# Kernel tuning notes

Measured on AMD Instinct MI355X. Metric: run time of the kernel, lower is better.

## Reference

```python
import jax, jax.numpy as jnp
import numpy as np

B, C, H, W = 8, 256, 64, 64
GROUPS = 32
EPS = 1e-6


def setup_inputs() -> dict:
    key = jax.random.key(0)
    ks = jax.random.split(key, 8)
    s = 0.02
    return {
        "x": jax.random.normal(ks[0], (B, C, H, W), dtype=jnp.float32),
        "gn_scale": jnp.ones((C,), jnp.float32),
        "gn_bias": jnp.zeros((C,), jnp.float32),
        "wq": jax.random.normal(ks[1], (C, C), jnp.float32) * s,
        "bq": jnp.zeros((C,), jnp.float32),
        "wk": jax.random.normal(ks[2], (C, C), jnp.float32) * s,
        "bk": jnp.zeros((C,), jnp.float32),
        "wv": jax.random.normal(ks[3], (C, C), jnp.float32) * s,
        "bv": jnp.zeros((C,), jnp.float32),
        "wproj": jax.random.normal(ks[4], (C, C), jnp.float32) * s,
        "bproj": jnp.zeros((C,), jnp.float32),
    }


def _group_norm(x, scale, bias):
    b, c, h, w = x.shape
    xg = x.reshape(b, GROUPS, c // GROUPS, h, w)
    mean = xg.mean(axis=(2, 3, 4), keepdims=True)
    var = xg.var(axis=(2, 3, 4), keepdims=True)
    xn = ((xg - mean) * jax.lax.rsqrt(var + EPS)).reshape(b, c, h, w)
    return xn * scale[None, :, None, None] + bias[None, :, None, None]


def _conv1x1(x, w, b):
    # 1x1 conv == channel-mixing matmul: w is [out_ch, in_ch]
    return jnp.einsum("oc,bchw->bohw", w, x) + b[None, :, None, None]


def reference(x, gn_scale, gn_bias, wq, bq, wk, bk, wv, bv, wproj, bproj):
    b, c, h, w = x.shape
    hn = _group_norm(x, gn_scale, gn_bias)
    q = _conv1x1(hn, wq, bq).reshape(b, c, h * w)  # [b,c,n]
    k = _conv1x1(hn, wk, bk).reshape(b, c, h * w)
    v = _conv1x1(hn, wv, bv).reshape(b, c, h * w)
    # scores[b,n,m] = <q[:, :, n], k[:, :, m]> * c^-0.5  (softmax over keys m)
    scale = jnp.asarray(c, x.dtype) ** -0.5
    attn = jax.nn.softmax(jnp.einsum("bcn,bcm->bnm", q, k) * scale, axis=2)
    # h_[b,c,n] = sum_m v[b,c,m] * attn[b,n,m]
    h_ = jnp.einsum("bcm,bnm->bcn", v, attn).reshape(b, c, h, w)
    h_ = _conv1x1(h_, wproj, bproj)
    return x + h_
```

## Files before the change

### kernel.cpp

```cpp
#include <hip/hip_runtime.h>

#define B_ 8
#define C_ 256
#define N_ 4096
#define G_ 32

typedef __bf16 bf16;
typedef __bf16 bf16x8 __attribute__((ext_vector_type(8)));
typedef float f32x4 __attribute__((ext_vector_type(4)));
typedef float f32x16 __attribute__((ext_vector_type(16)));
typedef long i64;
typedef long i64x2 __attribute__((ext_vector_type(2)));
typedef long i64x2a __attribute__((ext_vector_type(2), may_alias));
typedef int i32x8 __attribute__((ext_vector_type(8)));
typedef int i32x8a __attribute__((ext_vector_type(8), may_alias));
typedef unsigned int u32;
typedef unsigned char u8;
typedef unsigned short u16;
typedef unsigned long long u64;

__device__ __forceinline__ f32x4 mfma16(bf16x8 a, bf16x8 b, f32x4 c) {
    return __builtin_amdgcn_mfma_f32_16x16x32_bf16(a, b, c, 0, 0, 0);
}
__device__ __forceinline__ f32x16 mfma_mx(i32x8 a, i32x8 b, f32x16 c) {
    return __builtin_amdgcn_mfma_scale_f32_32x32x64_f8f6f4(
        a, b, c, 0 , 0 , 0, 0x7F7F7F7F, 0, 0x7F7F7F7F);
}

typedef __attribute__((address_space(1))) const void* gas_t;
typedef __attribute__((address_space(3))) void* las_t;
__device__ __forceinline__ void gl2lds16(const void* g, void* l) {
    __builtin_amdgcn_global_load_lds((gas_t)g, (las_t)l, 16, 0, 0);
}

__device__ __forceinline__ float exp2_hw(float x) {
    return __builtin_amdgcn_exp2f(x);
}

__device__ __forceinline__ u32 f32_to_fp8(float x) {
    union { float f; u32 u; } c;
    c.f = x;
    u32 s = (c.u >> 24) & 0x80;
    u32 m = (c.u & 0x7fffffff) + 0x00080000;
    int e = (int)(m >> 23) - 127;
    if (e < -6) return s;
    if (e > 8) return s | 0x7e;
    u32 v = ((u32)(e + 7) << 3) | ((m >> 20) & 7);
    if (v > 0x7e) v = 0x7e;
    return s | v;
}
__device__ __forceinline__ u32 fp8_fast(float x) {
    union { float f; u32 u; } c;
    c.f = x;
    return ((c.u + 0x00080000u) >> 20) - 960u;
}
__device__ __forceinline__ u32 pk_fp8x4(float a, float b, float c, float d) {
#if __has_builtin(__builtin_amdgcn_cvt_pk_fp8_f32)
    int w = __builtin_amdgcn_cvt_pk_fp8_f32(a, b, 0, false);
    w = __builtin_amdgcn_cvt_pk_fp8_f32(c, d, w, true);
    return (u32)w;
#else
    return (fp8_fast(a) & 0xff) | ((fp8_fast(b) & 0xff) << 8) |
           ((fp8_fast(c) & 0xff) << 16) | (fp8_fast(d) << 24);
#endif
}

__global__ __launch_bounds__(256) void gn_part(const float* __restrict__ x,
                                               float* __restrict__ gpart) {
    int blk = blockIdx.x;
    int b = blk >> 8, g = (blk >> 3) & 31, qe = blk & 7;
    int tid = threadIdx.x;
    int c = g * 8 + (tid >> 5);
    const float* row = x + ((size_t)(b * C_ + c)) * N_ + qe * 512;
    float s = 0.f, s2 = 0.f;
    for (int n = (tid & 31) * 4; n < 512; n += 128) {
        float4 v = *(const float4*)(row + n);
        s += v.x + v.y + v.z + v.w;
        s2 += v.x * v.x + v.y * v.y + v.z * v.z + v.w * v.w;
    }
    for (int off = 32; off; off >>= 1) {
        s += __shfl_xor(s, off);
        s2 += __shfl_xor(s2, off);
    }
    __shared__ float red[8];
    int wid = tid >> 6;
    if ((tid & 63) == 0) { red[wid] = s; red[4 + wid] = s2; }
    __syncthreads();
    if (tid == 0) {
        gpart[blk * 2] = red[0] + red[1] + red[2] + red[3];
        gpart[blk * 2 + 1] = red[4] + red[5] + red[6] + red[7];
    }
}

__global__ __launch_bounds__(256) void gn_apply(const float* __restrict__ x,
                                                const float* __restrict__ gsc,
                                                const float* __restrict__ gbi,
                                                const float* __restrict__ gpart,
                                                bf16* __restrict__ hn) {
    __shared__ float tile[32][33];
    int b = blockIdx.z, c0 = blockIdx.y * 32, n0 = blockIdx.x * 32;
    int tx = threadIdx.x & 31, ty = threadIdx.x >> 5;
    for (int i = 0; i < 4; i++) {
        int cl = ty + i * 8;
        int c = c0 + cl;
        int g = c >> 3;
        const float* gp = gpart + ((size_t)(b * G_ + g)) * 16;
        float S = 0.f, S2 = 0.f;
#pragma unroll
        for (int j = 0; j < 8; j++) { S += gp[j * 2]; S2 += gp[j * 2 + 1]; }
        float mean = S * (1.f / 32768.f);
        float var = S2 * (1.f / 32768.f) - mean * mean;
        float rstd = rsqrtf(var + 1e-6f);
        float sc = gsc[c] * rstd;
        float bs = gbi[c] - mean * sc;
        float v = x[((size_t)(b * C_ + c)) * N_ + n0 + tx];
        tile[cl][tx] = v * sc + bs;
    }
    __syncthreads();
    for (int i = 0; i < 4; i++) {
        int nl = ty + i * 8;
        hn[((size_t)(b * N_ + n0 + nl)) * C_ + c0 + tx] = (bf16)tile[tx][nl];
    }
}

__global__ __launch_bounds__(256) void cvt_w(const float* __restrict__ wq,
                                             const float* __restrict__ wk,
                                             const float* __restrict__ wv,
                                             const float* __restrict__ wp,
                                             bf16* __restrict__ dst) {
    int i = blockIdx.x * 256 + threadIdx.x;
    dst[i] = (bf16)wq[i];
    dst[65536 + i] = (bf16)wk[i];
    dst[131072 + i] = (bf16)wv[i];
    dst[196608 + i] = (bf16)wp[i];
}

__global__ __launch_bounds__(256) void gemm_qkv(const bf16* __restrict__ A,
                                                const bf16* __restrict__ Wq,
                                                const bf16* __restrict__ Wk,
                                                const bf16* __restrict__ Wv,
                                                const float* __restrict__ bq,
                                                const float* __restrict__ bk,
                                                const float* __restrict__ bv,
                                                u8* __restrict__ q8,
                                                u8* __restrict__ k8,
                                                u8* __restrict__ v8) {
    __shared__ __align__(16) bf16 As[64][32];
    __shared__ __align__(16) bf16 Wqs[64][32];
    __shared__ __align__(16) bf16 Wks[64][32];
    __shared__ __align__(16) bf16 Wvs[64][32];
    int m0 = blockIdx.x * 64;
    int n0 = blockIdx.y * 64;
    int tid = threadIdx.x;
    int wv_ = tid >> 6, lane = tid & 63, lr = lane & 15, lq = lane >> 4;
    int wm = (wv_ & 1) * 32, wn = (wv_ >> 1) * 32;
    int sr = tid >> 2, sk = (tid & 3) * 8;
    f32x4 qacc[2][2] = {}, kacc[2][2] = {}, vacc[2][2] = {};
    for (int kk = 0; kk < C_; kk += 32) {
        __syncthreads();
        gl2lds16(&A[(size_t)(m0 + sr) * C_ + kk + sk], &As[sr][sk]);
        gl2lds16(&Wq[(size_t)(n0 + sr) * C_ + kk + sk], &Wqs[sr][sk]);
        gl2lds16(&Wk[(size_t)(n0 + sr) * C_ + kk + sk], &Wks[sr][sk]);
        gl2lds16(&Wv[(size_t)(n0 + sr) * C_ + kk + sk], &Wvs[sr][sk]);
        __syncthreads();
        bf16x8 a0 = *(const bf16x8*)&As[wm + lr][lq * 8];
        bf16x8 a1 = *(const bf16x8*)&As[wm + 16 + lr][lq * 8];
        bf16x8 q0 = *(const bf16x8*)&Wqs[wn + lr][lq * 8];
        bf16x8 q1 = *(const bf16x8*)&Wqs[wn + 16 + lr][lq * 8];
        bf16x8 k0 = *(const bf16x8*)&Wks[wn + lr][lq * 8];
        bf16x8 k1 = *(const bf16x8*)&Wks[wn + 16 + lr][lq * 8];
        bf16x8 v0 = *(const bf16x8*)&Wvs[wn + lr][lq * 8];
        bf16x8 v1 = *(const bf16x8*)&Wvs[wn + 16 + lr][lq * 8];
        qacc[0][0] = mfma16(a0, q0, qacc[0][0]);
        qacc[0][1] = mfma16(a0, q1, qacc[0][1]);
        qacc[1][0] = mfma16(a1, q0, qacc[1][0]);
        qacc[1][1] = mfma16(a1, q1, qacc[1][1]);
        kacc[0][0] = mfma16(a0, k0, kacc[0][0]);
        kacc[0][1] = mfma16(a0, k1, kacc[0][1]);
        kacc[1][0] = mfma16(a1, k0, kacc[1][0]);
        kacc[1][1] = mfma16(a1, k1, kacc[1][1]);
        vacc[0][0] = mfma16(a0, v0, vacc[0][0]);
        vacc[0][1] = mfma16(a0, v1, vacc[0][1]);
        vacc[1][0] = mfma16(a1, v0, vacc[1][0]);
        vacc[1][1] = mfma16(a1, v1, vacc[1][1]);
    }
    for (int i = 0; i < 2; i++)
        for (int j = 0; j < 2; j++) {
            int col = n0 + wn + j * 16 + lr;
            float bvq = bq[col], bvk = bk[col], bvv = bv[col];
            for (int r = 0; r < 4; r++) {
                int row = m0 + wm + i * 16 + lq * 4 + r;
                q8[(size_t)row * C_ + col] = (u8)f32_to_fp8(qacc[i][j][r] + bvq);
                k8[(size_t)row * C_ + col] = (u8)f32_to_fp8(kacc[i][j][r] + bvk);
                int bb = row >> 12, n = row & (N_ - 1);
                int h = (n >> 11) & 1, mtl = (n >> 6) & 31, k6 = n & 63;
                int hbv = (k6 >> 2) & 1;
                int jv = ((k6 >> 5) << 4) | (((k6 >> 3) & 3) << 2) | (k6 & 3);
                jv ^= ((col ^ hbv) & 1) << 4;
                v8[((size_t)(((bb * 2 + h) * 32 + mtl) * 2 + hbv)) * 8192 +
                   col * 32 + jv] = (u8)f32_to_fp8(vacc[i][j][r] + bvv);
            }
        }
}

__global__ __launch_bounds__(128, 2) void attn(const u8* __restrict__ q,
                                               const u8* __restrict__ k,
                                               const u8* __restrict__ vT,
                                               bf16* __restrict__ O0,
                                               bf16* __restrict__ O1,
                                               float* __restrict__ lp) {
    __shared__ __align__(16) u8 smem[40960];

    int flat = blockIdx.x + (blockIdx.y << 6) + (blockIdx.z << 7);
    int nid = (flat & 7) * 128 + (flat >> 3);
    int q0 = (nid & 63) * 64;
    int h = (nid >> 6) & 1;
    int b = nid >> 7;
    int tid = threadIdx.x;
    int w = tid >> 6, lane = tid & 63, lc = lane & 31, hb = lane >> 5;

    const u8* kglob = k + ((size_t)(b * N_) + h * 2048) * 256;
    const u8* vglob = vT + ((size_t)(b * 2 + h)) * 32 * 16384;

    u32 offK[4];
#pragma unroll
    for (int j = 0; j < 4; j++) {
        int p = j * 128 + tid;
        offK[j] = (u32)((p >> 4) * 256 + (((p & 15) ^ ((p >> 4) & 15)) << 4));
    }

    const u8* qrow = q + ((size_t)(b * N_ + q0 + w * 32 + lc)) * 256 + hb * 32;
    i32x8 qf[4];
#pragma unroll
    for (int kh = 0; kh < 4; kh++) qf[kh] = *(const i32x8a*)&qrow[kh * 64];

    f32x16 oacc[8] = {};
    f32x16 eacc = {};
    u32 swz = (u32)(lc & 15);
    u32 vsw0 = (u32)(((lc ^ hb) & 1) << 4);

    auto STAGE_K = [&](int sidx, int buf) {
        const u8* kg = kglob + (size_t)sidx * 8192;
        u8* dst = smem + buf * 8192;
#pragma unroll
        for (int j = 0; j < 4; j++)
            gl2lds16(kg + offK[j], dst + (j * 128 + tid) * 16);
    };
    auto STAGE_V = [&](int t) {
        const u8* vg = vglob + (size_t)t * 16384;
#pragma unroll
        for (int j = 0; j < 8; j++)
            gl2lds16(vg + (j * 128 + tid) * 16, smem + 24576 + (j * 128 + tid) * 16);
    };

    STAGE_K(0, 0);
    STAGE_K(1, 1);
    STAGE_V(0);

    for (int mt = 0; mt < 32; mt++) {
        int bufa = (2 * mt) % 3, bufb = (2 * mt + 1) % 3, bufc = (2 * mt + 2) % 3;
        if (mt < 31) {
            STAGE_K(2 * mt + 2, bufc);
            asm volatile("s_waitcnt vmcnt(4)" ::: "memory");
        } else {
            asm volatile("s_waitcnt vmcnt(0)" ::: "memory");
        }
        __builtin_amdgcn_s_barrier();

        const u8* Ka = smem + bufa * 8192;
        const u8* Kb = smem + bufb * 8192;
        __builtin_amdgcn_s_setprio(1);

        f32x16 st0 = {}, st1 = {};
#pragma unroll
        for (int kh = 0; kh < 4; kh++) {
            u32 g0 = (u32)(kh * 4 + hb * 2);
            union { i64x2 h2[2]; i32x8 v; } kf0, kf1;
            kf0.h2[0] = *(const i64x2a*)&Ka[lc * 256 + ((g0 ^ swz) << 4)];
            kf0.h2[1] = *(const i64x2a*)&Ka[lc * 256 + (((g0 + 1) ^ swz) << 4)];
            st0 = mfma_mx(kf0.v, qf[kh], st0);
            kf1.h2[0] = *(const i64x2a*)&Kb[lc * 256 + ((g0 ^ swz) << 4)];
            kf1.h2[1] = *(const i64x2a*)&Kb[lc * 256 + (((g0 + 1) ^ swz) << 4)];
            st1 = mfma_mx(kf1.v, qf[kh], st1);
        }

        f32x16 e0, e1;
#pragma unroll
        for (int i = 0; i < 16; i++) {
            e0[i] = exp2_hw(st0[i] * (1.44269504089f * 0.0625f));
            e1[i] = exp2_hw(st1[i] * (1.44269504089f * 0.0625f));
        }
        eacc += e0;
        eacc += e1;
        i32x8 pf;
#pragma unroll
        for (int t4 = 0; t4 < 4; t4++) {
            pf[t4] = (int)pk_fp8x4(e0[t4 * 4], e0[t4 * 4 + 1], e0[t4 * 4 + 2],
                                   e0[t4 * 4 + 3]);
            pf[4 + t4] = (int)pk_fp8x4(e1[t4 * 4], e1[t4 * 4 + 1], e1[t4 * 4 + 2],
                                       e1[t4 * 4 + 3]);
        }

        const u8* Vb = smem + 24576;
#pragma unroll
        for (int ct = 0; ct < 8; ct++) {
            u32 base = (u32)(hb * 8192 + (ct * 32 + lc) * 32);
            union { i64x2 h2[2]; i32x8 v; } vf;
            vf.h2[0] = *(const i64x2a*)&Vb[base + vsw0];
            vf.h2[1] = *(const i64x2a*)&Vb[base + (vsw0 ^ 16)];
            oacc[ct] = mfma_mx(pf, vf.v, oacc[ct]);
        }
        __builtin_amdgcn_s_setprio(0);

        if (mt < 31) {
            asm volatile("s_waitcnt lgkmcnt(0)" ::: "memory");
            __builtin_amdgcn_s_barrier();
            STAGE_K(2 * mt + 3, bufa);
            STAGE_V(mt + 1);
        }
    }

    float hs = 0.f;
#pragma unroll
    for (int i = 0; i < 16; i++) hs += eacc[i];
    float lsum = hs + __shfl_xor(hs, 32);

    bf16* Op = h ? O1 : O0;
#pragma unroll
    for (int ct = 0; ct < 8; ct++)
#pragma unroll
        for (int r = 0; r < 16; r++) {
            int qq = (r & 3) + hb * 4 + (r >> 2) * 8;
            Op[((size_t)(b * N_ + q0 + w * 32 + qq)) * C_ + ct * 32 + lc] =
                (bf16)oacc[ct][r];
        }
    if (hb == 0)
        lp[((size_t)(h * B_ + b)) * N_ + q0 + w * 32 + lc] = lsum;
}

__global__ __launch_bounds__(256) void proj_res(const bf16* __restrict__ W,
                                                const bf16* __restrict__ O0,
                                                const bf16* __restrict__ O1,
                                                const float* __restrict__ lp,
                                                const float* __restrict__ bias,
                                                const float* __restrict__ x,
                                                float* __restrict__ out) {
    __shared__ __align__(16) bf16 Ws[256][32];
    __shared__ __align__(16) bf16 As[64][32];
    int n0 = blockIdx.x * 64;
    int tid = threadIdx.x;
    int wv_ = tid >> 6, lane = tid & 63, lr = lane & 15, lq = lane >> 4;
    int wm = (wv_ & 1) * 32;
    int wn = (wv_ >> 1) * 32;
    int sr = tid >> 2, sk = (tid & 3) * 8;
    int T = n0 + sr, bb = T >> 12, nn = T & (N_ - 1);
    float inv = 1.f / (lp[(size_t)bb * N_ + nn] + lp[(size_t)(B_ + bb) * N_ + nn]);
    f32x4 acc[4][2][2] = {};
    for (int kk = 0; kk < C_; kk += 32) {
        __syncthreads();
#pragma unroll
        for (int p = 0; p < 4; p++)
            gl2lds16(&W[(size_t)(p * 64 + sr) * C_ + kk + sk], &Ws[p * 64 + sr][sk]);
        bf16x8 o0 = *(const bf16x8*)&O0[(size_t)T * C_ + kk + sk];
        bf16x8 o1 = *(const bf16x8*)&O1[(size_t)T * C_ + kk + sk];
        bf16x8 cm;
#pragma unroll
        for (int e = 0; e < 8; e++) cm[e] = (bf16)(((float)o0[e] + (float)o1[e]) * inv);
        *(bf16x8*)&As[sr][sk] = cm;
        __syncthreads();
        bf16x8 a0 = *(const bf16x8*)&As[wm + lr][lq * 8];
        bf16x8 a1 = *(const bf16x8*)&As[wm + 16 + lr][lq * 8];
#pragma unroll
        for (int ot = 0; ot < 4; ot++) {
            bf16x8 w0 = *(const bf16x8*)&Ws[ot * 64 + wn + lr][lq * 8];
            bf16x8 w1 = *(const bf16x8*)&Ws[ot * 64 + wn + 16 + lr][lq * 8];
            acc[ot][0][0] = mfma16(w0, a0, acc[ot][0][0]);
            acc[ot][0][1] = mfma16(w0, a1, acc[ot][0][1]);
            acc[ot][1][0] = mfma16(w1, a0, acc[ot][1][0]);
            acc[ot][1][1] = mfma16(w1, a1, acc[ot][1][1]);
        }
    }
#pragma unroll
    for (int ot = 0; ot < 4; ot++)
        for (int i = 0; i < 2; i++)
            for (int j = 0; j < 2; j++) {
                int Tt = n0 + wm + j * 16 + lr;
                int b = Tt >> 12, n = Tt & (N_ - 1);
                for (int r = 0; r < 4; r++) {
                    int o = ot * 64 + wn + i * 16 + lq * 4 + r;
                    size_t idx = ((size_t)(b * C_ + o)) * N_ + n;
                    out[idx] = x[idx] + acc[ot][i][j][r] + bias[o];
                }
            }
}

extern "C" void kernel_launch(void* const* d_in, const int* in_sizes, int n_in,
                              void* d_out, int out_size, void* d_ws, size_t ws_size,
                              hipStream_t stream) {
    const float* x = (const float*)d_in[0];
    const float* gsc = (const float*)d_in[1];
    const float* gbi = (const float*)d_in[2];
    const float* wq = (const float*)d_in[3];
    const float* bq = (const float*)d_in[4];
    const float* wk = (const float*)d_in[5];
    const float* bk = (const float*)d_in[6];
    const float* wv = (const float*)d_in[7];
    const float* bv = (const float*)d_in[8];
    const float* wp = (const float*)d_in[9];
    const float* bp = (const float*)d_in[10];
    float* out = (float*)d_out;

    const size_t SZ = (size_t)B_ * N_ * C_;
    char* ws = (char*)d_ws;
    bf16* wb = (bf16*)(ws + 4096);
    char* base = ws + 4096 + 524288;
    bf16* hn = (bf16*)base;
    u8* q8 = (u8*)(base + SZ * 2);
    u8* k8 = (u8*)(base + SZ * 3);
    u8* v8 = (u8*)(base + SZ * 4);
    bf16* O0 = (bf16*)base;
    bf16* O1 = (bf16*)(base + SZ * 5);
    float* gpart = (float*)(base + SZ * 7);
    float* lpart = (float*)(base + SZ * 7);

    cvt_w<<<256, 256, 0, stream>>>(wq, wk, wv, wp, wb);
    gn_part<<<B_ * G_ * 8, 256, 0, stream>>>(x, gpart);
    gn_apply<<<dim3(N_ / 32, C_ / 32, B_), 256, 0, stream>>>(x, gsc, gbi, gpart, hn);
    gemm_qkv<<<dim3(B_ * N_ / 64, C_ / 64), 256, 0, stream>>>(
        hn, wb, wb + 65536, wb + 131072, bq, bk, bv, q8, k8, v8);
    attn<<<dim3(N_ / 64, 2, B_), 128, 0, stream>>>(q8, k8, v8, O0, O1, lpart);
    proj_res<<<B_ * N_ / 64, 256, 0, stream>>>(
        wb + 196608, O0, O1, lpart, bp, x, out);
}
```

Before: 255.4 us.

## Load V fragments directly from global memory and software-pipeline PV across iterations

```diff
diff --git a/kernel.cpp b/kernel.cpp
--- a/kernel.cpp
+++ b/kernel.cpp
@@ -37,18 +37,6 @@
     return __builtin_amdgcn_exp2f(x);
 }
 
-__device__ __forceinline__ u32 f32_to_fp8(float x) {
-    union { float f; u32 u; } c;
-    c.f = x;
-    u32 s = (c.u >> 24) & 0x80;
-    u32 m = (c.u & 0x7fffffff) + 0x00080000;
-    int e = (int)(m >> 23) - 127;
-    if (e < -6) return s;
-    if (e > 8) return s | 0x7e;
-    u32 v = ((u32)(e + 7) << 3) | ((m >> 20) & 7);
-    if (v > 0x7e) v = 0x7e;
-    return s | v;
-}
 __device__ __forceinline__ u32 fp8_fast(float x) {
     union { float f; u32 u; } c;
     c.f = x;
@@ -188,17 +176,22 @@
         for (int j = 0; j < 2; j++) {
             int col = n0 + wn + j * 16 + lr;
             float bvq = bq[col], bvk = bk[col], bvv = bv[col];
+            u32 qw = pk_fp8x4(qacc[i][j][0] + bvq, qacc[i][j][1] + bvq,
+                              qacc[i][j][2] + bvq, qacc[i][j][3] + bvq);
+            u32 kw = pk_fp8x4(kacc[i][j][0] + bvk, kacc[i][j][1] + bvk,
+                              kacc[i][j][2] + bvk, kacc[i][j][3] + bvk);
+            u32 vw = pk_fp8x4(vacc[i][j][0] + bvv, vacc[i][j][1] + bvv,
+                              vacc[i][j][2] + bvv, vacc[i][j][3] + bvv);
             for (int r = 0; r < 4; r++) {
                 int row = m0 + wm + i * 16 + lq * 4 + r;
-                q8[(size_t)row * C_ + col] = (u8)f32_to_fp8(qacc[i][j][r] + bvq);
-                k8[(size_t)row * C_ + col] = (u8)f32_to_fp8(kacc[i][j][r] + bvk);
+                q8[(size_t)row * C_ + col] = (u8)(qw >> (8 * r));
+                k8[(size_t)row * C_ + col] = (u8)(kw >> (8 * r));
                 int bb = row >> 12, n = row & (N_ - 1);
                 int h = (n >> 11) & 1, mtl = (n >> 6) & 31, k6 = n & 63;
                 int hbv = (k6 >> 2) & 1;
                 int jv = ((k6 >> 5) << 4) | (((k6 >> 3) & 3) << 2) | (k6 & 3);
-                jv ^= ((col ^ hbv) & 1) << 4;
                 v8[((size_t)(((bb * 2 + h) * 32 + mtl) * 2 + hbv)) * 8192 +
-                   col * 32 + jv] = (u8)f32_to_fp8(vacc[i][j][r] + bvv);
+                   col * 32 + jv] = (u8)(vw >> (8 * r));
             }
         }
 }
@@ -209,7 +202,7 @@
                                                bf16* __restrict__ O0,
                                                bf16* __restrict__ O1,
                                                float* __restrict__ lp) {
-    __shared__ __align__(16) u8 smem[40960];
+    __shared__ __align__(16) u8 smem[24576];
 
     int flat = blockIdx.x + (blockIdx.y << 6) + (blockIdx.z << 7);
     int nid = (flat & 7) * 128 + (flat >> 3);
@@ -220,7 +213,7 @@
     int w = tid >> 6, lane = tid & 63, lc = lane & 31, hb = lane >> 5;
 
     const u8* kglob = k + ((size_t)(b * N_) + h * 2048) * 256;
-    const u8* vglob = vT + ((size_t)(b * 2 + h)) * 32 * 16384;
+    const u8* vglob = vT + ((size_t)(b * 2 + h)) * 32 * 16384 + hb * 8192 + lc * 32;
 
     u32 offK[4];
 #pragma unroll
@@ -237,7 +230,6 @@
     f32x16 oacc[8] = {};
     f32x16 eacc = {};
     u32 swz = (u32)(lc & 15);
-    u32 vsw0 = (u32)(((lc ^ hb) & 1) << 4);
 
     auto STAGE_K = [&](int sidx, int buf) {
         const u8* kg = kglob + (size_t)sidx * 8192;
@@ -246,17 +238,11 @@
         for (int j = 0; j < 4; j++)
             gl2lds16(kg + offK[j], dst + (j * 128 + tid) * 16);
     };
-    auto STAGE_V = [&](int t) {
-        const u8* vg = vglob + (size_t)t * 16384;
-#pragma unroll
-        for (int j = 0; j < 8; j++)
-            gl2lds16(vg + (j * 128 + tid) * 16, smem + 24576 + (j * 128 + tid) * 16);
-    };
 
     STAGE_K(0, 0);
     STAGE_K(1, 1);
-    STAGE_V(0);
-
+
+    i32x8 pfA = {};
     for (int mt = 0; mt < 32; mt++) {
         int bufa = (2 * mt) % 3, bufb = (2 * mt + 1) % 3, bufc = (2 * mt + 2) % 3;
         if (mt < 31) {
@@ -284,6 +270,16 @@
             st1 = mfma_mx(kf1.v, qf[kh], st1);
         }
 
+        if (mt) {
+            const u8* Vb = vglob + (size_t)(mt - 1) * 16384;
+            i32x8 vr[8];
+#pragma unroll
+            for (int ct = 0; ct < 8; ct++) vr[ct] = *(const i32x8a*)&Vb[ct * 1024];
+#pragma unroll
+            for (int ct = 0; ct < 8; ct++)
+                oacc[ct] = mfma_mx(pfA, vr[ct], oacc[ct]);
+        }
+
         f32x16 e0, e1;
 #pragma unroll
         for (int i = 0; i < 16; i++) {
@@ -292,23 +288,12 @@
         }
         eacc += e0;
         eacc += e1;
-        i32x8 pf;
 #pragma unroll
         for (int t4 = 0; t4 < 4; t4++) {
-            pf[t4] = (int)pk_fp8x4(e0[t4 * 4], e0[t4 * 4 + 1], e0[t4 * 4 + 2],
-                                   e0[t4 * 4 + 3]);
-            pf[4 + t4] = (int)pk_fp8x4(e1[t4 * 4], e1[t4 * 4 + 1], e1[t4 * 4 + 2],
-                                       e1[t4 * 4 + 3]);
-        }
-
-        const u8* Vb = smem + 24576;
-#pragma unroll
-        for (int ct = 0; ct < 8; ct++) {
-            u32 base = (u32)(hb * 8192 + (ct * 32 + lc) * 32);
-            union { i64x2 h2[2]; i32x8 v; } vf;
-            vf.h2[0] = *(const i64x2a*)&Vb[base + vsw0];
-            vf.h2[1] = *(const i64x2a*)&Vb[base + (vsw0 ^ 16)];
-            oacc[ct] = mfma_mx(pf, vf.v, oacc[ct]);
+            pfA[t4] = (int)pk_fp8x4(e0[t4 * 4], e0[t4 * 4 + 1], e0[t4 * 4 + 2],
+                                    e0[t4 * 4 + 3]);
+            pfA[4 + t4] = (int)pk_fp8x4(e1[t4 * 4], e1[t4 * 4 + 1], e1[t4 * 4 + 2],
+                                        e1[t4 * 4 + 3]);
         }
         __builtin_amdgcn_s_setprio(0);
 
@@ -316,7 +301,15 @@
             asm volatile("s_waitcnt lgkmcnt(0)" ::: "memory");
             __builtin_amdgcn_s_barrier();
             STAGE_K(2 * mt + 3, bufa);
-            STAGE_V(mt + 1);
+        }
+    }
+
+    {
+        const u8* Vb = vglob + (size_t)31 * 16384;
+#pragma unroll
+        for (int ct = 0; ct < 8; ct++) {
+            i32x8 vf = *(const i32x8a*)&Vb[ct * 1024];
+            oacc[ct] = mfma_mx(pfA, vf, oacc[ct]);
         }
     }
 
```

After: 305.0 us. 19.4% more time.
